# Optimization experiments

Measured on AMD Instinct MI355X. Metric: run time of the kernel, lower is better.

## Reference

```python
import jax, jax.numpy as jnp
import numpy as np

B, L, C = 2, 8192, 256
K, NLEV = 17, 4
HALF = K // 2


def setup_inputs() -> dict:
    key = jax.random.key(0)
    ks = jax.random.split(key, 10)
    s = 0.02
    return {
        "x": jax.random.normal(ks[0], (B, L, C), jnp.float32),
        "stem_w": jax.random.normal(ks[1], (C, C, 2), jnp.float32) * s,   # Conv1d (out,in,k)
        "stem_b": jax.random.normal(ks[2], (C,), jnp.float32) * s,
        "qkv_w": jax.random.normal(ks[3], (3 * C, C), jnp.float32) * s,
        "width_w": jax.random.normal(ks[4], (1, C), jnp.float32) * s,
        "width_b": jax.random.normal(ks[5], (1,), jnp.float32) * s,
        "out_w": jax.random.normal(ks[6], (C, C), jnp.float32) * s,
        "query": jax.random.normal(ks[7], (NLEV * C,), jnp.float32) * s,
        "film_w": jax.random.normal(ks[8], (2 * C, NLEV * C), jnp.float32) * s,
        "film_b": jax.random.normal(ks[9], (2 * C,), jnp.float32) * s,
    }


def _local_attn(h, qkv_w, width_w, width_b, out_w):
    # h: (b, l, c); 1D local windowed attention with learned sigmoid distance mask
    b, l, c = h.shape
    rel_dist = jnp.abs(jnp.arange(K, dtype=h.dtype) - HALF)  # (K,)
    max_dist = float(HALF)
    scale = c ** -0.5
    qkv = h @ qkv_w.T
    q, k, v = jnp.split(qkv, 3, axis=-1)
    width = jax.nn.sigmoid(h @ width_w.T + width_b) * max_dist + 0.5  # (b,l,1)
    k_pad = jnp.pad(k, ((0, 0), (HALF, HALF), (0, 0)))
    v_pad = jnp.pad(v, ((0, 0), (HALF, HALF), (0, 0)))
    idx = jnp.arange(l)[:, None] + jnp.arange(K)[None, :]  # (l,K) indices into padded seq
    k_win = k_pad[:, idx]  # (b,l,K,c)
    v_win = v_pad[:, idx]  # (b,l,K,c)
    scores = jnp.einsum('blc,blwc->blw', q, k_win) * scale
    soft_mask = jax.nn.sigmoid((width - rel_dist) * 5.0)  # (b,l,K)
    scores = scores - (1.0 - soft_mask) * 10000.0
    attn = jax.nn.softmax(scores, axis=-1)
    o = jnp.einsum('blw,blwc->blc', attn, v_win)
    return (o + v) @ out_w.T


def _forward(x, stem_w, stem_b, qkv_w, width_w, width_b, out_w, query, film_w, film_b):
    b, l, c = x.shape
    # stem conv: Conv1d(C, C, kernel=2, padding=1), then narrow to first l positions
    h = jnp.transpose(x, (0, 2, 1))  # (B,C,L)
    h = jax.lax.conv_general_dilated(h, stem_w, (1,), [(1, 1)],
                                     dimension_numbers=('NCH', 'OIH', 'NCH'))
    h = h[:, :, :l] + stem_b[None, :, None]
    h = jnp.transpose(h, (0, 2, 1))  # (B,L,C)
    levels = []
    for i in range(NLEV):
        h = _local_attn(h, qkv_w, width_w, width_b, out_w)
        levels.append(h)
        if i < NLEV - 1:  # avg_pool(kernel=2, stride=2)
            bl = h.shape[1]
            h = h.reshape(b, bl // 2, 2, c).mean(axis=2)
    # nearest upsample each coarser level back to L (factors are exact powers of 2)
    ups = [levels[0]]
    for lvl in levels[1:]:
        ups.append(jnp.repeat(lvl, l // lvl.shape[1], axis=1))
    concat = jnp.concatenate(ups, axis=-1)  # (B,L,NLEV*C)
    gattn = jax.nn.softmax(concat @ query, axis=-1)  # (B,L)
    global_ctx = jnp.einsum('bl,bld->bd', gattn, concat)  # (B,NLEV*C)
    film = global_ctx @ film_w.T + film_b  # (B,2C)
    scale_f, bias_f = jnp.split(film, 2, axis=-1)
    return levels[0] * (1.0 + scale_f[:, None, :]) + bias_f[:, None, :]


def reference(x, stem_w, stem_b, qkv_w, width_w, width_b, out_w, query, film_w, film_b):
    return _forward(x, stem_w, stem_b, qkv_w, width_w, width_b, out_w, query, film_w, film_b)
```

## Files before the change

### kernel.cpp

```cpp
#include <hip/hip_runtime.h>
#include <math.h>

#define L_SEQ 8192
#define B_SZ  2
#define CH    256
#define NLEV  4

typedef __attribute__((ext_vector_type(8))) short bf16x8;
typedef __attribute__((ext_vector_type(4))) float f32x4;

static __device__ __forceinline__ float sigmoidf_(float x) {
    return 1.0f / (1.0f + expf(-x));
}

static __device__ __forceinline__ float bf2f_(unsigned short u) {
    union { unsigned int ui; float f; } x;
    x.ui = ((unsigned int)u) << 16;
    return x.f;
}
static __device__ __forceinline__ unsigned short f2b_(float f) {
    union { float f; unsigned int u; } x;
    x.f = f;
    unsigned int lsb = (x.u >> 16) & 1u;
    unsigned int r = x.u + 0x7fffu + lsb;
    return (unsigned short)(r >> 16);
}
static __device__ __forceinline__ float4 ldb4_(const unsigned short* p) {
    ushort4 u = *(const ushort4*)p;
    return make_float4(bf2f_(u.x), bf2f_(u.y), bf2f_(u.z), bf2f_(u.w));
}

__global__ void prep_kernel(const float* __restrict__ x,
                            const float* __restrict__ qkv_w,
                            const float* __restrict__ out_w,
                            const float* __restrict__ stem_w,
                            unsigned short* __restrict__ x16g,
                            unsigned short* __restrict__ qw16,
                            unsigned short* __restrict__ ow16,
                            unsigned short* __restrict__ sw16)
{
    int i = blockIdx.x * 256 + threadIdx.x;
    if (i < 256) { x16g[i] = 0; return; }
    i -= 256;
    if (i < 4194304) { x16g[256 + i] = f2b_(x[i]); return; }
    i -= 4194304;
    if (i < 196608) { qw16[i] = f2b_(qkv_w[i]); return; }
    i -= 196608;
    if (i < 65536) { ow16[i] = f2b_(out_w[i]); return; }
    i -= 65536;
    {
        int k = i & 511, n = i >> 9;
        float v = (k < 256) ? stem_w[(size_t)n * 512 + k * 2]
                            : stem_w[(size_t)n * 512 + (k - 256) * 2 + 1];
        sw16[i] = f2b_(v);
    }
}

__global__ __launch_bounds__(256) void wvp_fold(
    const float* __restrict__ ow, const float* __restrict__ qkvw,
    unsigned short* __restrict__ qw16)
{
    __shared__ float owr[256];
    const int c = blockIdx.x, j = threadIdx.x;
    owr[j] = ow[(size_t)c * 256 + j];
    __syncthreads();
    float acc = 0.0f;
    #pragma unroll 8
    for (int k = 0; k < 256; ++k)
        acc += owr[k] * qkvw[(size_t)(512 + k) * 256 + j];
    qw16[(size_t)(512 + c) * 256 + j] = f2b_(acc);
}

__global__ __launch_bounds__(256) void stem_gemm_bf16(
    const unsigned short* __restrict__ x16g, const unsigned short* __restrict__ W,
    unsigned short* __restrict__ outB, const float* __restrict__ bias)
{
    __shared__ unsigned short As[128 * 32];
    __shared__ unsigned short Bs[128 * 32];
    const int tid  = threadIdx.x;
    const int wave = tid >> 6;
    const int lane = tid & 63;
    const int bm = blockIdx.y * 128;
    const int bn = blockIdx.x * 128;
    const int wm = (wave & 1) * 64;
    const int wn = (wave >> 1) * 64;
    const int srow = lane >> 2;
    const int scol = (lane & 3) * 8;

    f32x4 acc[4][4] = {};

    for (int k0 = 0; k0 < 512; k0 += 32) {
        __syncthreads();
        #pragma unroll
        for (int c = 0; c < 2; ++c) {
            const int chunk = c * 4 + wave;
            const int row = bm + chunk * 16 + srow;
            const int t = row & (L_SEQ - 1);
            const unsigned short* ga;
            if (k0 < 256)
                ga = x16g + (t > 0 ? (size_t)row * 256 : 0) + k0 + scol;
            else
                ga = x16g + ((size_t)row + 1) * 256 + (k0 - 256) + scol;
            const unsigned short* gw = W + (size_t)(bn + chunk * 16 + srow) * 512 + k0 + scol;
            __builtin_amdgcn_global_load_lds(
                (const __attribute__((address_space(1))) void*)ga,
                (__attribute__((address_space(3))) void*)(As + chunk * 16 * 32),
                16, 0, 0);
            __builtin_amdgcn_global_load_lds(
                (const __attribute__((address_space(1))) void*)gw,
                (__attribute__((address_space(3))) void*)(Bs + chunk * 16 * 32),
                16, 0, 0);
        }
        __syncthreads();

        bf16x8 af[4], bf[4];
        const int fr = lane & 15;
        const int kk = (lane >> 4) * 8;
        #pragma unroll
        for (int i = 0; i < 4; ++i) {
            af[i] = *(const bf16x8*)(As + (wm + i * 16 + fr) * 32 + kk);
            bf[i] = *(const bf16x8*)(Bs + (wn + i * 16 + fr) * 32 + kk);
        }
        #pragma unroll
        for (int i = 0; i < 4; ++i)
            #pragma unroll
            for (int j = 0; j < 4; ++j)
                acc[i][j] = __builtin_amdgcn_mfma_f32_16x16x32_bf16(
                    af[i], bf[j], acc[i][j], 0, 0, 0);
    }

    const int cn = lane & 15;
    const int cr = (lane >> 4) * 4;
    #pragma unroll
    for (int i = 0; i < 4; ++i)
        #pragma unroll
        for (int r = 0; r < 4; ++r) {
            const int m = bm + wm + i * 16 + cr + r;
            #pragma unroll
            for (int j = 0; j < 4; ++j) {
                const int n = bn + wn + j * 16 + cn;
                outB[(size_t)m * CH + n] = f2b_(acc[i][j][r] + bias[n]);
            }
        }
}

__global__ __launch_bounds__(256) void gemm_bf16(
    const unsigned short* __restrict__ A, const unsigned short* __restrict__ W,
    unsigned short* __restrict__ outB, int M, int N, int Kd)
{
    __shared__ unsigned short As[128 * 32];
    __shared__ unsigned short Bs[128 * 32];
    const int tid  = threadIdx.x;
    const int wave = tid >> 6;
    const int lane = tid & 63;
    const int bm = blockIdx.y * 128;
    const int bn = blockIdx.x * 128;
    const int wm = (wave & 1) * 64;
    const int wn = (wave >> 1) * 64;
    const int srow = lane >> 2;
    const int scol = (lane & 3) * 8;

    f32x4 acc[4][4] = {};

    for (int k0 = 0; k0 < Kd; k0 += 32) {
        __syncthreads();
        #pragma unroll
        for (int c = 0; c < 2; ++c) {
            const int chunk = c * 4 + wave;
            const int row = chunk * 16 + srow;
            const unsigned short* ga = A + (size_t)(bm + row) * Kd + k0 + scol;
            const unsigned short* gw = W + (size_t)(bn + row) * Kd + k0 + scol;
            __builtin_amdgcn_global_load_lds(
                (const __attribute__((address_space(1))) void*)ga,
                (__attribute__((address_space(3))) void*)(As + chunk * 16 * 32),
                16, 0, 0);
            __builtin_amdgcn_global_load_lds(
                (const __attribute__((address_space(1))) void*)gw,
                (__attribute__((address_space(3))) void*)(Bs + chunk * 16 * 32),
                16, 0, 0);
        }
        __syncthreads();

        bf16x8 af[4], bf[4];
        const int fr = lane & 15;
        const int kk = (lane >> 4) * 8;
        #pragma unroll
        for (int i = 0; i < 4; ++i) {
            af[i] = *(const bf16x8*)(As + (wm + i * 16 + fr) * 32 + kk);
            bf[i] = *(const bf16x8*)(Bs + (wn + i * 16 + fr) * 32 + kk);
        }
        #pragma unroll
        for (int i = 0; i < 4; ++i)
            #pragma unroll
            for (int j = 0; j < 4; ++j)
                acc[i][j] = __builtin_amdgcn_mfma_f32_16x16x32_bf16(
                    af[i], bf[j], acc[i][j], 0, 0, 0);
    }

    const int cn = lane & 15;
    const int cr = (lane >> 4) * 4;
    #pragma unroll
    for (int i = 0; i < 4; ++i)
        #pragma unroll
        for (int r = 0; r < 4; ++r) {
            const int m = bm + wm + i * 16 + cr + r;
            const size_t rowoff = (size_t)m * N;
            #pragma unroll
            for (int j = 0; j < 4; ++j)
                outB[rowoff + bn + wn + j * 16 + cn] = f2b_(acc[i][j][r]);
        }
}

__global__ __launch_bounds__(256) void attn_vp_kernel(
    const unsigned short* __restrict__ qkv, const unsigned short* __restrict__ h16,
    const float* __restrict__ ww, const float* __restrict__ wbp,
    unsigned short* __restrict__ l16o, unsigned short* __restrict__ dsB, int l)
{
    __shared__ __align__(16) unsigned short vt[256 * 88];
    __shared__ __align__(16) unsigned short pb[4 * 512];

    const int tid  = threadIdx.x;
    const int wave = tid >> 6;
    const int lane = tid & 63;
    const int q    = lane >> 4;
    const int n    = lane & 15;

    int bid = blockIdx.x;
    const int cpx = gridDim.x >> 3;
    bid = (bid & 7) * cpx + (bid >> 3);

    const int bps = l >> 6;
    const int b  = bid / bps;
    const int t0 = (bid % bps) << 6;
    const size_t seqbase = (size_t)b * l;
    const int row0 = t0 + wave * 16;

    bf16x8 vval[10];
    {
        const int r = tid & 15;
        const int ch0 = tid >> 4;
        #pragma unroll
        for (int p5 = 0; p5 < 5; ++p5)
            #pragma unroll
            for (int cc = 0; cc < 2; ++cc) {
                const int grow = t0 - 8 + p5 * 16 + r;
                bf16x8 val = {0, 0, 0, 0, 0, 0, 0, 0};
                if (grow >= 0 && grow < l)
                    val = *(const bf16x8*)(qkv + (seqbase + grow) * 768 + 512 +
                                           (cc * 16 + ch0) * 8);
                vval[p5 * 2 + cc] = val;
            }
    }

    float wdot = 0.0f;
    {
        const unsigned short* hrow = h16 + (seqbase + row0 + n) * 256 + q * 64;
        #pragma unroll
        for (int jj = 0; jj < 8; ++jj) {
            bf16x8 hv = *(const bf16x8*)(hrow + jj * 8);
            float4 wa = *((const float4*)(ww + q * 64 + jj * 8));
            float4 wc = *((const float4*)(ww + q * 64 + jj * 8 + 4));
            wdot += bf2f_(((unsigned short*)&hv)[0]) * wa.x
                  + bf2f_(((unsigned short*)&hv)[1]) * wa.y
                  + bf2f_(((unsigned short*)&hv)[2]) * wa.z
                  + bf2f_(((unsigned short*)&hv)[3]) * wa.w
                  + bf2f_(((unsigned short*)&hv)[4]) * wc.x
                  + bf2f_(((unsigned short*)&hv)[5]) * wc.y
                  + bf2f_(((unsigned short*)&hv)[6]) * wc.z
                  + bf2f_(((unsigned short*)&hv)[7]) * wc.w;
        }
    }
    wdot += __shfl_xor(wdot, 16, 64);
    wdot += __shfl_xor(wdot, 32, 64);
    const float w_n = sigmoidf_(wdot + wbp[0]) * 8.0f + 0.5f;

    bf16x8 qf[8];
    const unsigned short* qrow = qkv + (seqbase + row0 + n) * 768;
    #pragma unroll
    for (int kk = 0; kk < 8; ++kk)
        qf[kk] = *(const bf16x8*)(qrow + kk * 32 + q * 8);

    f32x4 accS[2] = {};
    #pragma unroll
    for (int h = 0; h < 2; ++h) {
        const int grow = row0 - 8 + h * 16 + n;
        const bool ok = (grow >= 0 && grow < l);
        const unsigned short* kb = qkv + (seqbase + grow) * 768 + 256 + q * 8;
        #pragma unroll
        for (int kk = 0; kk < 8; ++kk) {
            bf16x8 bk = {0, 0, 0, 0, 0, 0, 0, 0};
            if (ok) bk = *(const bf16x8*)(kb + kk * 32);
            accS[h] = __builtin_amdgcn_mfma_f32_16x16x32_bf16(
                qf[kk], bk, accS[h], 0, 0, 0);
        }
    }

    {
        const int r = tid & 15;
        const int ch0 = tid >> 4;
        #pragma unroll
        for (int p5 = 0; p5 < 5; ++p5)
            #pragma unroll
            for (int cc = 0; cc < 2; ++cc) {
                const int rr = p5 * 16 + r;
                const int chunk = cc * 16 + ch0;
                #pragma unroll
                for (int jj = 0; jj < 8; ++jj)
                    vt[(chunk * 8 + jj) * 88 + rr] =
                        ((unsigned short*)&vval[p5 * 2 + cc])[jj];
            }
    }

    float wd[4];
    #pragma unroll
    for (int r = 0; r < 4; ++r) wd[r] = __shfl(w_n, q * 4 + r, 64);

    float s[2][4];
    #pragma unroll
    for (int h = 0; h < 2; ++h)
        #pragma unroll
        for (int r = 0; r < 4; ++r) {
            int ii = q * 4 + r;
            int c  = h * 16 + n;
            int w  = c - ii;
            float dist = fabsf((float)w - 8.0f);
            float sm = sigmoidf_((wd[r] - dist) * 5.0f);
            float v = accS[h][r] * 0.0625f - (1.0f - sm) * 10000.0f;
            s[h][r] = (w >= 0 && w <= 16) ? v : -3.0e38f;
        }

    float mx[4], sum[4];
    #pragma unroll
    for (int r = 0; r < 4; ++r) mx[r] = fmaxf(s[0][r], s[1][r]);
    #pragma unroll
    for (int m = 1; m < 16; m <<= 1)
        #pragma unroll
        for (int r = 0; r < 4; ++r) mx[r] = fmaxf(mx[r], __shfl_xor(mx[r], m, 64));
    float e[2][4];
    #pragma unroll
    for (int h = 0; h < 2; ++h)
        #pragma unroll
        for (int r = 0; r < 4; ++r) e[h][r] = expf(s[h][r] - mx[r]);
    #pragma unroll
    for (int r = 0; r < 4; ++r) sum[r] = e[0][r] + e[1][r];
    #pragma unroll
    for (int m = 1; m < 16; m <<= 1)
        #pragma unroll
        for (int r = 0; r < 4; ++r) sum[r] += __shfl_xor(sum[r], m, 64);

    #pragma unroll
    for (int h = 0; h < 2; ++h)
        #pragma unroll
        for (int r = 0; r < 4; ++r) {
            int ii = q * 4 + r, c = h * 16 + n;
            float p = e[h][r] / sum[r];
            if (c == ii + 8) p += 1.0f;
            pb[wave * 512 + ii * 32 + c] = f2b_(p);
        }

    __syncthreads();

    bf16x8 pf = *(const bf16x8*)(pb + wave * 512 + n * 32 + q * 8);
    const int rl = q * 4;
    const size_t gbase = seqbase + row0;
    #pragma unroll
    for (int ct = 0; ct < 16; ++ct) {
        bf16x8 vf = *(const bf16x8*)(vt + (ct * 16 + n) * 88 + wave * 16 + q * 8);
        f32x4 z = {};
        f32x4 o = __builtin_amdgcn_mfma_f32_16x16x32_bf16(pf, vf, z, 0, 0, 0);
        const int col = ct * 16 + n;
        float v0 = o[0], v1 = o[1], v2 = o[2], v3 = o[3];
        size_t r0 = (gbase + rl) * CH + col;
        l16o[r0]          = f2b_(v0);
        l16o[r0 + CH]     = f2b_(v1);
        l16o[r0 + 2 * CH] = f2b_(v2);
        l16o[r0 + 3 * CH] = f2b_(v3);
        if (dsB) {
            size_t d0 = ((gbase + rl) >> 1) * CH + col;
            dsB[d0]      = f2b_(0.5f * (v0 + v1));
            dsB[d0 + CH] = f2b_(0.5f * (v2 + v3));
        }
    }
}

__global__ __launch_bounds__(1024) void tail_ctx_kernel(
    const unsigned short* __restrict__ l0, const unsigned short* __restrict__ l1,
    const unsigned short* __restrict__ l2, const unsigned short* __restrict__ l3,
    const float* __restrict__ query, float* __restrict__ partials,
    float* __restrict__ denomP)
{
    __shared__ float eS[128];
    const int tid = threadIdx.x;
    const int chunk = blockIdx.x, b = blockIdx.y;
    const int t0 = chunk * 128;
    const unsigned short* levp[4] = {l0, l1, l2, l3};

    const int w = tid >> 6, lane = tid & 63;
    const int lev = lane >> 4, c0 = (lane & 15) * 16;
    const unsigned short* lpbase = levp[lev] + (size_t)b * (L_SEQ >> lev) * CH;
    const float* qp = query + lev * CH + c0;
    float4 q0 = *(const float4*)(qp);
    float4 q1 = *(const float4*)(qp + 4);
    float4 q2 = *(const float4*)(qp + 8);
    float4 q3 = *(const float4*)(qp + 12);
    #pragma unroll
    for (int j = 0; j < 8; ++j) {
        int t = t0 + w * 8 + j;
        const unsigned short* p = lpbase + (size_t)(t >> lev) * CH + c0;
        float4 h0 = ldb4_(p), h1 = ldb4_(p + 4), h2 = ldb4_(p + 8), h3 = ldb4_(p + 12);
        float part = h0.x * q0.x + h0.y * q0.y + h0.z * q0.z + h0.w * q0.w
                   + h1.x * q1.x + h1.y * q1.y + h1.z * q1.z + h1.w * q1.w
                   + h2.x * q2.x + h2.y * q2.y + h2.z * q2.z + h2.w * q2.w
                   + h3.x * q3.x + h3.y * q3.y + h3.z * q3.z + h3.w * q3.w;
        #pragma unroll
        for (int m = 1; m < 64; m <<= 1) part += __shfl_xor(part, m, 64);
        if (lane == 0) eS[w * 8 + j] = expf(part);
    }
    __syncthreads();

    if (tid == 0) {
        float ds = 0.0f;
        #pragma unroll 8
        for (int i = 0; i < 128; ++i) ds += eS[i];
        denomP[b * 64 + chunk] = ds;
    }

    const int dlev = tid >> 8, c = tid & 255;
    const unsigned short* lp = levp[dlev] + (size_t)b * (L_SEQ >> dlev) * CH;
    float acc = 0.0f;
    #pragma unroll 4
    for (int t = t0; t < t0 + 128; ++t)
        acc += eS[t - t0] * bf2f_(lp[(size_t)(t >> dlev) * CH + c]);
    partials[(size_t)(b * 64 + chunk) * 1024 + tid] = acc;
}

__global__ __launch_bounds__(256) void ctx_reduce_kernel(
    const float* __restrict__ partials, const float* __restrict__ denomP,
    float* __restrict__ ctx)
{
    const int b = blockIdx.y;
    const int d = blockIdx.x * 256 + threadIdx.x;
    float acc = 0.0f;
    #pragma unroll
    for (int c = 0; c < 64; ++c) acc += partials[(size_t)(b * 64 + c) * 1024 + d];
    float den = 0.0f;
    #pragma unroll
    for (int c = 0; c < 64; ++c) den += denomP[b * 64 + c];
    ctx[b * 1024 + d] = acc / den;
}

__global__ __launch_bounds__(256) void film_kernel(
    const float* __restrict__ ctx, const float* __restrict__ fw,
    const float* __restrict__ fb, float* __restrict__ film)
{
    const int lane = threadIdx.x & 63;
    const int j = blockIdx.x * 4 + (threadIdx.x >> 6);
    float acc0 = 0.0f, acc1 = 0.0f;
    #pragma unroll
    for (int r = 0; r < 4; ++r) {
        float4 w4 = *((const float4*)(fw + (size_t)j * 1024 + r * 256) + lane);
        float4 c0 = *((const float4*)(ctx + r * 256) + lane);
        float4 c1 = *((const float4*)(ctx + 1024 + r * 256) + lane);
        acc0 += w4.x * c0.x + w4.y * c0.y + w4.z * c0.z + w4.w * c0.w;
        acc1 += w4.x * c1.x + w4.y * c1.y + w4.z * c1.z + w4.w * c1.w;
    }
    #pragma unroll
    for (int m = 1; m < 64; m <<= 1) {
        acc0 += __shfl_xor(acc0, m, 64);
        acc1 += __shfl_xor(acc1, m, 64);
    }
    if (lane == 0) {
        float b = fb[j];
        film[j] = acc0 + b;
        film[512 + j] = acc1 + b;
    }
}

__global__ void final_kernel(const unsigned short* __restrict__ lev0,
                             const float* __restrict__ film,
                             float* __restrict__ out)
{
    size_t n4 = ((size_t)blockIdx.x * 256 + threadIdx.x) * 4;
    int c = (int)(n4 & (CH - 1));
    int b = (int)(n4 >> 21);
    float4 h = ldb4_(lev0 + n4);
    const float* fs = film + b * 512;
    float4 o;
    o.x = h.x * (1.0f + fs[c + 0]) + fs[256 + c + 0];
    o.y = h.y * (1.0f + fs[c + 1]) + fs[256 + c + 1];
    o.z = h.z * (1.0f + fs[c + 2]) + fs[256 + c + 2];
    o.w = h.w * (1.0f + fs[c + 3]) + fs[256 + c + 3];
    *(float4*)(out + n4) = o;
}

extern "C" void kernel_launch(void* const* d_in, const int* in_sizes, int n_in,
                              void* d_out, int out_size, void* d_ws, size_t ws_size,
                              hipStream_t stream) {
    const float* x       = (const float*)d_in[0];
    const float* stem_w  = (const float*)d_in[1];
    const float* stem_b  = (const float*)d_in[2];
    const float* qkv_w   = (const float*)d_in[3];
    const float* width_w = (const float*)d_in[4];
    const float* width_b = (const float*)d_in[5];
    const float* out_w   = (const float*)d_in[6];
    const float* query   = (const float*)d_in[7];
    const float* film_w  = (const float*)d_in[8];
    const float* film_b  = (const float*)d_in[9];
    float* out = (float*)d_out;
    float* ws  = (float*)d_ws;

    float* partials = ws;
    float* denomP   = partials + 131072;
    float* ctx      = denomP + 128;
    float* film     = ctx + 2048;
    unsigned short* x16g  = (unsigned short*)(film + 1024);
    unsigned short* h16_0 = x16g + 4194560;
    unsigned short* h16_1 = h16_0 + 4194304;
    unsigned short* h16_2 = h16_1 + 2097152;
    unsigned short* h16_3 = h16_2 + 1048576;
    unsigned short* qkv16 = h16_3 + 524288;
    unsigned short* ov16  = qkv16 + 12582912;
    unsigned short* l16_0 = ov16 + 4194304;
    unsigned short* l16_1 = l16_0 + 4194304;
    unsigned short* l16_2 = l16_1 + 2097152;
    unsigned short* l16_3 = l16_2 + 1048576;
    unsigned short* qw16  = l16_3 + 524288;
    unsigned short* ow16  = qw16 + 196608;
    unsigned short* sw16  = ow16 + 65536;
    unsigned short* h16[4]  = {h16_0, h16_1, h16_2, h16_3};
    unsigned short* l16[4]  = {l16_0, l16_1, l16_2, l16_3};
    (void)ov16;

    prep_kernel<<<(256 + 4194304 + 196608 + 65536 + 131072) / 256, 256, 0, stream>>>(
        x, qkv_w, out_w, stem_w, x16g, qw16, ow16, sw16);

    wvp_fold<<<256, 256, 0, stream>>>(out_w, qkv_w, qw16);

    stem_gemm_bf16<<<dim3(CH / 128, B_SZ * L_SEQ / 128), 256, 0, stream>>>(
        x16g, sw16, h16_0, stem_b);

    for (int i = 0; i < NLEV; ++i) {
        const int l = L_SEQ >> i;
        const int M = B_SZ * l;
        gemm_bf16<<<dim3(768 / 128, M / 128), 256, 0, stream>>>(
            h16[i], qw16, qkv16, M, 768, CH);
        attn_vp_kernel<<<M / 64, 256, 0, stream>>>(
            qkv16, h16[i], width_w, width_b,
            l16[i], (i < NLEV - 1) ? h16[i + 1] : nullptr, l);
    }

    tail_ctx_kernel<<<dim3(64, B_SZ), 1024, 0, stream>>>(
        l16_0, l16_1, l16_2, l16_3, query, partials, denomP);
    ctx_reduce_kernel<<<dim3(4, B_SZ), 256, 0, stream>>>(partials, denomP, ctx);
    film_kernel<<<128, 256, 0, stream>>>(ctx, film_w, film_b, film);
    final_kernel<<<(B_SZ * L_SEQ * CH) / 1024, 256, 0, stream>>>(l16_0, film, out);
}
```

Baseline: 253.4 us.

## Split attention-value work across 16 waves per block and raise MFMA priority

```diff
diff --git a/kernel.cpp b/kernel.cpp
--- a/kernel.cpp
+++ b/kernel.cpp
@@ -211,7 +211,7 @@
         }
 }
 
-__global__ __launch_bounds__(256) void attn_vp_kernel(
+__global__ __launch_bounds__(1024) void attn_vp_kernel(
     const unsigned short* __restrict__ qkv, const unsigned short* __restrict__ h16,
     const float* __restrict__ ww, const float* __restrict__ wbp,
     unsigned short* __restrict__ l16o, unsigned short* __restrict__ dsB, int l)
@@ -222,6 +222,8 @@
     const int tid  = threadIdx.x;
     const int wave = tid >> 6;
     const int lane = tid & 63;
+    const int rt   = wave >> 2;
+    const int qt   = wave & 3;
     const int q    = lane >> 4;
     const int n    = lane & 15;
 
@@ -233,23 +235,20 @@
     const int b  = bid / bps;
     const int t0 = (bid % bps) << 6;
     const size_t seqbase = (size_t)b * l;
-    const int row0 = t0 + wave * 16;
-
-    bf16x8 vval[10];
-    {
-        const int r = tid & 15;
-        const int ch0 = tid >> 4;
-        #pragma unroll
-        for (int p5 = 0; p5 < 5; ++p5)
-            #pragma unroll
-            for (int cc = 0; cc < 2; ++cc) {
-                const int grow = t0 - 8 + p5 * 16 + r;
-                bf16x8 val = {0, 0, 0, 0, 0, 0, 0, 0};
-                if (grow >= 0 && grow < l)
-                    val = *(const bf16x8*)(qkv + (seqbase + grow) * 768 + 512 +
-                                           (cc * 16 + ch0) * 8);
-                vval[p5 * 2 + cc] = val;
-            }
+    const int row0 = t0 + rt * 16;
+
+    bf16x8 vval[3];
+    #pragma unroll
+    for (int i = 0; i < 3; ++i) {
+        const int tk = tid + i * 1024;
+        bf16x8 val = {0, 0, 0, 0, 0, 0, 0, 0};
+        if (tk < 2560) {
+            const int r = tk >> 5, ch = tk & 31;
+            const int grow = t0 - 8 + r;
+            if (grow >= 0 && grow < l)
+                val = *(const bf16x8*)(qkv + (seqbase + grow) * 768 + 512 + ch * 8);
+        }
+        vval[i] = val;
     }
 
     float wdot = 0.0f;
@@ -281,6 +280,7 @@
         qf[kk] = *(const bf16x8*)(qrow + kk * 32 + q * 8);
 
     f32x4 accS[2] = {};
+    __builtin_amdgcn_s_setprio(1);
     #pragma unroll
     for (int h = 0; h < 2; ++h) {
         const int grow = row0 - 8 + h * 16 + n;
@@ -294,21 +294,17 @@
                 qf[kk], bk, accS[h], 0, 0, 0);
         }
     }
-
-    {
-        const int r = tid & 15;
-        const int ch0 = tid >> 4;
-        #pragma unroll
-        for (int p5 = 0; p5 < 5; ++p5)
+    __builtin_amdgcn_s_setprio(0);
+
+    #pragma unroll
+    for (int i = 0; i < 3; ++i) {
+        const int tk = tid + i * 1024;
+        if (tk < 2560) {
+            const int r = tk >> 5, ch = tk & 31;
             #pragma unroll
-            for (int cc = 0; cc < 2; ++cc) {
-                const int rr = p5 * 16 + r;
-                const int chunk = cc * 16 + ch0;
-                #pragma unroll
-                for (int jj = 0; jj < 8; ++jj)
-                    vt[(chunk * 8 + jj) * 88 + rr] =
-                        ((unsigned short*)&vval[p5 * 2 + cc])[jj];
-            }
+            for (int jj = 0; jj < 8; ++jj)
+                vt[(ch * 8 + jj) * 88 + r] = ((unsigned short*)&vval[i])[jj];
+        }
     }
 
     float wd[4];
@@ -348,28 +344,38 @@
         #pragma unroll
         for (int r = 0; r < 4; ++r) sum[r] += __shfl_xor(sum[r], m, 64);
 
-    #pragma unroll
-    for (int h = 0; h < 2; ++h)
-        #pragma unroll
-        for (int r = 0; r < 4; ++r) {
-            int ii = q * 4 + r, c = h * 16 + n;
-            float p = e[h][r] / sum[r];
-            if (c == ii + 8) p += 1.0f;
-            pb[wave * 512 + ii * 32 + c] = f2b_(p);
-        }
+    if (qt == 0) {
+        #pragma unroll
+        for (int h = 0; h < 2; ++h)
+            #pragma unroll
+            for (int r = 0; r < 4; ++r) {
+                int ii = q * 4 + r, c = h * 16 + n;
+                float p = e[h][r] / sum[r];
+                if (c == ii + 8) p += 1.0f;
+                pb[rt * 512 + ii * 32 + c] = f2b_(p);
+            }
+    }
 
     __syncthreads();
 
-    bf16x8 pf = *(const bf16x8*)(pb + wave * 512 + n * 32 + q * 8);
+    bf16x8 pf = *(const bf16x8*)(pb + rt * 512 + n * 32 + q * 8);
     const int rl = q * 4;
     const size_t gbase = seqbase + row0;
-    #pragma unroll
-    for (int ct = 0; ct < 16; ++ct) {
-        bf16x8 vf = *(const bf16x8*)(vt + (ct * 16 + n) * 88 + wave * 16 + q * 8);
+    __builtin_amdgcn_s_setprio(1);
+    f32x4 po[4];
+    #pragma unroll
+    for (int c = 0; c < 4; ++c) {
+        const int ct = qt * 4 + c;
+        bf16x8 vf = *(const bf16x8*)(vt + (ct * 16 + n) * 88 + rt * 16 + q * 8);
         f32x4 z = {};
-        f32x4 o = __builtin_amdgcn_mfma_f32_16x16x32_bf16(pf, vf, z, 0, 0, 0);
+        po[c] = __builtin_amdgcn_mfma_f32_16x16x32_bf16(pf, vf, z, 0, 0, 0);
+    }
+    __builtin_amdgcn_s_setprio(0);
+    #pragma unroll
+    for (int c = 0; c < 4; ++c) {
+        const int ct = qt * 4 + c;
         const int col = ct * 16 + n;
-        float v0 = o[0], v1 = o[1], v2 = o[2], v3 = o[3];
+        float v0 = po[c][0], v1 = po[c][1], v2 = po[c][2], v3 = po[c][3];
         size_t r0 = (gbase + rl) * CH + col;
         l16o[r0]          = f2b_(v0);
         l16o[r0 + CH]     = f2b_(v1);
@@ -544,7 +550,7 @@
         const int M = B_SZ * l;
         gemm_bf16<<<dim3(768 / 128, M / 128), 256, 0, stream>>>(
             h16[i], qw16, qkv16, M, 768, CH);
-        attn_vp_kernel<<<M / 64, 256, 0, stream>>>(
+        attn_vp_kernel<<<M / 64, 1024, 0, stream>>>(
             qkv16, h16[i], width_w, width_b,
             l16[i], (i < NLEV - 1) ? h16[i + 1] : nullptr, l);
     }
```

Result: slower. 314.9 us (+24.3%).

## Merge weight-fold into prep kernel and hoist attention loads ahead of compute

Applied to the files above, without the earlier changes.

```diff
diff --git a/kernel.cpp b/kernel.cpp
--- a/kernel.cpp
+++ b/kernel.cpp
@@ -30,45 +30,38 @@
     return make_float4(bf2f_(u.x), bf2f_(u.y), bf2f_(u.z), bf2f_(u.w));
 }
 
-__global__ void prep_kernel(const float* __restrict__ x,
-                            const float* __restrict__ qkv_w,
-                            const float* __restrict__ out_w,
-                            const float* __restrict__ stem_w,
-                            unsigned short* __restrict__ x16g,
-                            unsigned short* __restrict__ qw16,
-                            unsigned short* __restrict__ ow16,
-                            unsigned short* __restrict__ sw16)
-{
+#define NPREP_BLOCKS 17409
+__global__ __launch_bounds__(256) void prep_kernel(
+    const float* __restrict__ x, const float* __restrict__ qkv_w,
+    const float* __restrict__ out_w, const float* __restrict__ stem_w,
+    unsigned short* __restrict__ x16g, unsigned short* __restrict__ qw16,
+    unsigned short* __restrict__ sw16)
+{
+    __shared__ float owr[256];
+    if (blockIdx.x >= NPREP_BLOCKS) {
+        const int c = blockIdx.x - NPREP_BLOCKS, j = threadIdx.x;
+        owr[j] = out_w[(size_t)c * 256 + j];
+        __syncthreads();
+        float acc = 0.0f;
+        #pragma unroll 8
+        for (int k = 0; k < 256; ++k)
+            acc += owr[k] * qkv_w[(size_t)(512 + k) * 256 + j];
+        qw16[(size_t)(512 + c) * 256 + j] = f2b_(acc);
+        return;
+    }
     int i = blockIdx.x * 256 + threadIdx.x;
     if (i < 256) { x16g[i] = 0; return; }
     i -= 256;
     if (i < 4194304) { x16g[256 + i] = f2b_(x[i]); return; }
     i -= 4194304;
-    if (i < 196608) { qw16[i] = f2b_(qkv_w[i]); return; }
-    i -= 196608;
-    if (i < 65536) { ow16[i] = f2b_(out_w[i]); return; }
-    i -= 65536;
+    if (i < 131072) { qw16[i] = f2b_(qkv_w[i]); return; }
+    i -= 131072;
     {
-        int k = i & 511, n = i >> 9;
-        float v = (k < 256) ? stem_w[(size_t)n * 512 + k * 2]
-                            : stem_w[(size_t)n * 512 + (k - 256) * 2 + 1];
+        int k = i & 511, nn = i >> 9;
+        float v = (k < 256) ? stem_w[(size_t)nn * 512 + k * 2]
+                            : stem_w[(size_t)nn * 512 + (k - 256) * 2 + 1];
         sw16[i] = f2b_(v);
     }
-}
-
-__global__ __launch_bounds__(256) void wvp_fold(
-    const float* __restrict__ ow, const float* __restrict__ qkvw,
-    unsigned short* __restrict__ qw16)
-{
-    __shared__ float owr[256];
-    const int c = blockIdx.x, j = threadIdx.x;
-    owr[j] = ow[(size_t)c * 256 + j];
-    __syncthreads();
-    float acc = 0.0f;
-    #pragma unroll 8
-    for (int k = 0; k < 256; ++k)
-        acc += owr[k] * qkvw[(size_t)(512 + k) * 256 + j];
-    qw16[(size_t)(512 + c) * 256 + j] = f2b_(acc);
 }
 
 __global__ __launch_bounds__(256) void stem_gemm_bf16(
@@ -211,7 +204,7 @@
         }
 }
 
-__global__ __launch_bounds__(256) void attn_vp_kernel(
+__global__ __launch_bounds__(256, 1) void attn_vp_kernel(
     const unsigned short* __restrict__ qkv, const unsigned short* __restrict__ h16,
     const float* __restrict__ ww, const float* __restrict__ wbp,
     unsigned short* __restrict__ l16o, unsigned short* __restrict__ dsB, int l)
@@ -235,6 +228,30 @@
     const size_t seqbase = (size_t)b * l;
     const int row0 = t0 + wave * 16;
 
+    bf16x8 hv[8];
+    {
+        const unsigned short* hrow = h16 + (seqbase + row0 + n) * 256 + q * 64;
+        #pragma unroll
+        for (int jj = 0; jj < 8; ++jj) hv[jj] = *(const bf16x8*)(hrow + jj * 8);
+    }
+    bf16x8 qf[8];
+    {
+        const unsigned short* qrow = qkv + (seqbase + row0 + n) * 768 + q * 8;
+        #pragma unroll
+        for (int kk = 0; kk < 8; ++kk) qf[kk] = *(const bf16x8*)(qrow + kk * 32);
+    }
+    bf16x8 bk[2][8];
+    #pragma unroll
+    for (int h = 0; h < 2; ++h) {
+        const int grow = row0 - 8 + h * 16 + n;
+        const bool ok = (grow >= 0 && grow < l);
+        const unsigned short* kb = qkv + (seqbase + grow) * 768 + 256 + q * 8;
+        #pragma unroll
+        for (int kk = 0; kk < 8; ++kk) {
+            bf16x8 z = {0, 0, 0, 0, 0, 0, 0, 0};
+            bk[h][kk] = ok ? *(const bf16x8*)(kb + kk * 32) : z;
+        }
+    }
     bf16x8 vval[10];
     {
         const int r = tid & 15;
@@ -251,49 +268,80 @@
                 vval[p5 * 2 + cc] = val;
             }
     }
+    __builtin_amdgcn_sched_barrier(0);
 
     float wdot = 0.0f;
-    {
-        const unsigned short* hrow = h16 + (seqbase + row0 + n) * 256 + q * 64;
-        #pragma unroll
-        for (int jj = 0; jj < 8; ++jj) {
-            bf16x8 hv = *(const bf16x8*)(hrow + jj * 8);
-            float4 wa = *((const float4*)(ww + q * 64 + jj * 8));
-            float4 wc = *((const float4*)(ww + q * 64 + jj * 8 + 4));
-            wdot += bf2f_(((unsigned short*)&hv)[0]) * wa.x
-                  + bf2f_(((unsigned short*)&hv)[1]) * wa.y
-                  + bf2f_(((unsigned short*)&hv)[2]) * wa.z
-                  + bf2f_(((unsigned short*)&hv)[3]) * wa.w
-                  + bf2f_(((unsigned short*)&hv)[4]) * wc.x
-                  + bf2f_(((unsigned short*)&hv)[5]) * wc.y
-                  + bf2f_(((unsigned short*)&hv)[6]) * wc.z
-                  + bf2f_(((unsigned short*)&hv)[7]) * wc.w;
-        }
+    #pragma unroll
+    for (int jj = 0; jj < 8; ++jj) {
+        float4 wa = *((const float4*)(ww + q * 64 + jj * 8));
+        float4 wc = *((const float4*)(ww + q * 64 + jj * 8 + 4));
+        wdot += bf2f_((unsigned short)hv[jj][0]) * wa.x
+              + bf2f_((unsigned short)hv[jj][1]) * wa.y
+              + bf2f_((unsigned short)hv[jj][2]) * wa.z
+              + bf2f_((unsigned short)hv[jj][3]) * wa.w
+              + bf2f_((unsigned short)hv[jj][4]) * wc.x
+              + bf2f_((unsigned short)hv[jj][5]) * wc.y
+              + bf2f_((unsigned short)hv[jj][6]) * wc.z
+              + bf2f_((unsigned short)hv[jj][7]) * wc.w;
     }
     wdot += __shfl_xor(wdot, 16, 64);
     wdot += __shfl_xor(wdot, 32, 64);
     const float w_n = sigmoidf_(wdot + wbp[0]) * 8.0f + 0.5f;
 
-    bf16x8 qf[8];
-    const unsigned short* qrow = qkv + (seqbase + row0 + n) * 768;
-    #pragma unroll
-    for (int kk = 0; kk < 8; ++kk)
-        qf[kk] = *(const bf16x8*)(qrow + kk * 32 + q * 8);
-
     f32x4 accS[2] = {};
     #pragma unroll
-    for (int h = 0; h < 2; ++h) {
-        const int grow = row0 - 8 + h * 16 + n;
-        const bool ok = (grow >= 0 && grow < l);
-        const unsigned short* kb = qkv + (seqbase + grow) * 768 + 256 + q * 8;
-        #pragma unroll
-        for (int kk = 0; kk < 8; ++kk) {
-            bf16x8 bk = {0, 0, 0, 0, 0, 0, 0, 0};
-            if (ok) bk = *(const bf16x8*)(kb + kk * 32);
+    for (int h = 0; h < 2; ++h)
+        #pragma unroll
+        for (int kk = 0; kk < 8; ++kk)
             accS[h] = __builtin_amdgcn_mfma_f32_16x16x32_bf16(
-                qf[kk], bk, accS[h], 0, 0, 0);
-        }
-    }
+                qf[kk], bk[h][kk], accS[h], 0, 0, 0);
+
+    float wd[4];
+    #pragma unroll
+    for (int r = 0; r < 4; ++r) wd[r] = __shfl(w_n, q * 4 + r, 64);
+
+    float s[2][4];
+    #pragma unroll
+    for (int h = 0; h < 2; ++h)
+        #pragma unroll
+        for (int r = 0; r < 4; ++r) {
+            int ii = q * 4 + r;
+            int c  = h * 16 + n;
+            int w  = c - ii;
+            float dist = fabsf((float)w - 8.0f);
+            float sm = sigmoidf_((wd[r] - dist) * 5.0f);
+            float v = accS[h][r] * 0.0625f - (1.0f - sm) * 10000.0f;
+            s[h][r] = (w >= 0 && w <= 16) ? v : -3.0e38f;
+        }
+
+    float mx[4], sum[4];
+    #pragma unroll
+    for (int r = 0; r < 4; ++r) mx[r] = fmaxf(s[0][r], s[1][r]);
+    #pragma unroll
+    for (int m = 1; m < 16; m <<= 1)
+        #pragma unroll
+        for (int r = 0; r < 4; ++r) mx[r] = fmaxf(mx[r], __shfl_xor(mx[r], m, 64));
+    float e[2][4];
+    #pragma unroll
+    for (int h = 0; h < 2; ++h)
+        #pragma unroll
+        for (int r = 0; r < 4; ++r) e[h][r] = expf(s[h][r] - mx[r]);
+    #pragma unroll
+    for (int r = 0; r < 4; ++r) sum[r] = e[0][r] + e[1][r];
+    #pragma unroll
+    for (int m = 1; m < 16; m <<= 1)
+        #pragma unroll
+        for (int r = 0; r < 4; ++r) sum[r] += __shfl_xor(sum[r], m, 64);
+
+    #pragma unroll
+    for (int h = 0; h < 2; ++h)
+        #pragma unroll
+        for (int r = 0; r < 4; ++r) {
+            int ii = q * 4 + r, c = h * 16 + n;
+            float p = e[h][r] / sum[r];
+            if (c == ii + 8) p += 1.0f;
+            pb[wave * 512 + ii * 32 + c] = f2b_(p);
+        }
 
     {
         const int r = tid & 15;
@@ -307,56 +355,9 @@
                 #pragma unroll
                 for (int jj = 0; jj < 8; ++jj)
                     vt[(chunk * 8 + jj) * 88 + rr] =
-                        ((unsigned short*)&vval[p5 * 2 + cc])[jj];
+                        (unsigned short)vval[p5 * 2 + cc][jj];
             }
     }
-
-    float wd[4];
-    #pragma unroll
-    for (int r = 0; r < 4; ++r) wd[r] = __shfl(w_n, q * 4 + r, 64);
-
-    float s[2][4];
-    #pragma unroll
-    for (int h = 0; h < 2; ++h)
-        #pragma unroll
-        for (int r = 0; r < 4; ++r) {
-            int ii = q * 4 + r;
-            int c  = h * 16 + n;
-            int w  = c - ii;
-            float dist = fabsf((float)w - 8.0f);
-            float sm = sigmoidf_((wd[r] - dist) * 5.0f);
-            float v = accS[h][r] * 0.0625f - (1.0f - sm) * 10000.0f;
-            s[h][r] = (w >= 0 && w <= 16) ? v : -3.0e38f;
-        }
-
-    float mx[4], sum[4];
-    #pragma unroll
-    for (int r = 0; r < 4; ++r) mx[r] = fmaxf(s[0][r], s[1][r]);
-    #pragma unroll
-    for (int m = 1; m < 16; m <<= 1)
-        #pragma unroll
-        for (int r = 0; r < 4; ++r) mx[r] = fmaxf(mx[r], __shfl_xor(mx[r], m, 64));
-    float e[2][4];
-    #pragma unroll
-    for (int h = 0; h < 2; ++h)
-        #pragma unroll
-        for (int r = 0; r < 4; ++r) e[h][r] = expf(s[h][r] - mx[r]);
-    #pragma unroll
-    for (int r = 0; r < 4; ++r) sum[r] = e[0][r] + e[1][r];
-    #pragma unroll
-    for (int m = 1; m < 16; m <<= 1)
-        #pragma unroll
-        for (int r = 0; r < 4; ++r) sum[r] += __shfl_xor(sum[r], m, 64);
-
-    #pragma unroll
-    for (int h = 0; h < 2; ++h)
-        #pragma unroll
-        for (int r = 0; r < 4; ++r) {
-            int ii = q * 4 + r, c = h * 16 + n;
-            float p = e[h][r] / sum[r];
-            if (c == ii + 8) p += 1.0f;
-            pb[wave * 512 + ii * 32 + c] = f2b_(p);
-        }
 
     __syncthreads();
 
@@ -529,12 +530,10 @@
     unsigned short* sw16  = ow16 + 65536;
     unsigned short* h16[4]  = {h16_0, h16_1, h16_2, h16_3};
     unsigned short* l16[4]  = {l16_0, l16_1, l16_2, l16_3};
-    (void)ov16;
-
-    prep_kernel<<<(256 + 4194304 + 196608 + 65536 + 131072) / 256, 256, 0, stream>>>(
-        x, qkv_w, out_w, stem_w, x16g, qw16, ow16, sw16);
-
-    wvp_fold<<<256, 256, 0, stream>>>(out_w, qkv_w, qw16);
+    (void)ov16; (void)ow16;
+
+    prep_kernel<<<NPREP_BLOCKS + 256, 256, 0, stream>>>(
+        x, qkv_w, out_w, stem_w, x16g, qw16, sw16);
 
     stem_gemm_bf16<<<dim3(CH / 128, B_SZ * L_SEQ / 128), 256, 0, stream>>>(
         x16g, sw16, h16_0, stem_b);
```

Result: no change. 249.0 us (-1.7%).
